# Kernel optimization log

Hardware: AMD Instinct MI355X
Metric: run time of the kernel (lower is better)

Reference implementation:

```python
import jax, jax.numpy as jnp
import numpy as np

NEG_SLOPE = 0.2  # PyG GATConv default negative_slope


def gat_layer(x, src, dst, W, a_src, a_dst, bias, concat, N):
    """PyG GATConv: h = xW; e_ij = LeakyReLU(a_src.h_j + a_dst.h_i);
    alpha = segment-softmax over incoming edges of i; out_i = sum_j alpha_ij h_j."""
    H, C = a_src.shape
    h = (x @ W).reshape(N, H, C)                      # [N,H,C]
    alpha_s = jnp.einsum('nhc,hc->nh', h, a_src)      # [N,H]
    alpha_d = jnp.einsum('nhc,hc->nh', h, a_dst)      # [N,H]
    e = jax.nn.leaky_relu(alpha_s[src] + alpha_d[dst], NEG_SLOPE)  # [E,H]
    # numerically-stable segment softmax over destination nodes
    m = jax.ops.segment_max(e, dst, num_segments=N)   # [N,H]
    e = jnp.exp(e - m[dst])
    denom = jax.ops.segment_sum(e, dst, num_segments=N)
    alpha = e / (denom[dst] + 1e-16)                  # [E,H]
    msg = h[src] * alpha[:, :, None]                  # [E,H,C]
    out = jax.ops.segment_sum(msg, dst, num_segments=N)  # [N,H,C]
    out = out.reshape(N, H * C) if concat else out.mean(axis=1)
    return out + bias


def setup_inputs() -> dict:
    key = jax.random.key(0)
    ks = jax.random.split(key, 12)
    N, E, F_IN, C, H = 50000, 800000, 512, 32, 8
    s = 0.05
    x = jax.random.normal(ks[0], (N, F_IN), dtype=jnp.float32)
    edge_index = jax.random.randint(ks[1], (2, E), 0, N, dtype=jnp.int64)
    W1 = jax.random.normal(ks[2], (F_IN, H * C), dtype=jnp.float32) * s
    as1 = jax.random.normal(ks[3], (H, C), dtype=jnp.float32) * s
    ad1 = jax.random.normal(ks[4], (H, C), dtype=jnp.float32) * s
    b1 = jnp.zeros((H * C,), dtype=jnp.float32)
    W2 = jax.random.normal(ks[5], (H * C, H * C), dtype=jnp.float32) * s
    as2 = jax.random.normal(ks[6], (H, C), dtype=jnp.float32) * s
    ad2 = jax.random.normal(ks[7], (H, C), dtype=jnp.float32) * s
    b2 = jnp.zeros((C,), dtype=jnp.float32)
    Wp = jax.random.normal(ks[8], (C, 1), dtype=jnp.float32) * s
    bp = jnp.zeros((1,), dtype=jnp.float32)
    return {"edge_index": edge_index, "x": x, "W1": W1, "as1": as1, "ad1": ad1,
            "b1": b1, "W2": W2, "as2": as2, "ad2": ad2, "b2": b2,
            "Wp": Wp, "bp": bp}


def reference(edge_index, x, W1, as1, ad1, b1, W2, as2, ad2, b2, Wp, bp):
    N = x.shape[0]
    # PyG GATConv adds self-loops by default
    loops = jnp.arange(N, dtype=edge_index.dtype)
    src = jnp.concatenate([edge_index[0], loops])
    dst = jnp.concatenate([edge_index[1], loops])
    h = gat_layer(x, src, dst, W1, as1, ad1, b1, concat=True, N=N)
    h = jax.nn.relu(h)
    # F.dropout(training=self.training) is identity in eval mode
    h = gat_layer(h, src, dst, W2, as2, ad2, b2, concat=False, N=N)
    return jax.nn.sigmoid(h @ Wp + bp)   # [N,1]
```

## Files before the change

### kernel.cpp

```cpp
#include <hip/hip_runtime.h>
#include <math.h>

#define H_HEADS 8
#define C_DIM   32
#define HC      256
#define F_IN    512
#define NEG_SLOPE 0.2f

typedef __attribute__((ext_vector_type(8))) short    bf16x8;
typedef __attribute__((ext_vector_type(4))) short    s16x4;
typedef __attribute__((ext_vector_type(4))) float    f32x4;
typedef __attribute__((ext_vector_type(2))) float    f32x2;

__device__ __forceinline__ short f2bf(float f) {
    union { float f; unsigned u; } v; v.f = f;
    unsigned r = v.u + 0x7FFF + ((v.u >> 16) & 1);
    return (short)(r >> 16);
}

__device__ __forceinline__ bf16x8 cvt8(float4 a, float4 b) {
    union { bf16x8 v; unsigned u[4]; } r;
    asm("v_cvt_pk_bf16_f32 %0, %1, %2" : "=v"(r.u[0]) : "v"(a.x), "v"(a.y));
    asm("v_cvt_pk_bf16_f32 %0, %1, %2" : "=v"(r.u[1]) : "v"(a.z), "v"(a.w));
    asm("v_cvt_pk_bf16_f32 %0, %1, %2" : "=v"(r.u[2]) : "v"(b.x), "v"(b.y));
    asm("v_cvt_pk_bf16_f32 %0, %1, %2" : "=v"(r.u[3]) : "v"(b.z), "v"(b.w));
    return r.v;
}

__device__ __forceinline__ void gl2lds16(const short* g, short* l) {
    __builtin_amdgcn_global_load_lds(
        (const __attribute__((address_space(1))) void*)g,
        (__attribute__((address_space(3))) void*)l, 16, 0, 0);
}

__global__ void wfrag_kernel(const float* __restrict__ W1, const float* __restrict__ W2,
                             short* __restrict__ Wf1, short* __restrict__ Wf2)
{
    const int NW1 = F_IN * HC;
    const int NW2 = HC * HC;
    int tid = blockIdx.x * 256 + threadIdx.x;
    const float* W; short* Wf; int t;
    if (tid < NW1)            { W = W1; Wf = Wf1; t = tid; }
    else if (tid < NW1 + NW2) { W = W2; Wf = Wf2; t = tid - NW1; }
    else return;
    int j  = t & 7;
    int l  = (t >> 3) & 63;
    int nb = (t >> 9) & 15;
    int s  = t >> 13;
    int k  = s * 32 + (l >> 4) * 8 + j;
    int n  = nb * 16 + (l & 15);
    Wf[t] = f2bf(W[(size_t)k * HC + n]);
}

template<bool ABF16>
__global__ __launch_bounds__(256) void gemm_mfma(const void* __restrict__ Aptr,
    const short* __restrict__ Bf, unsigned char* __restrict__ h8,
    const float* __restrict__ a_s, const float* __restrict__ a_d,
    float* __restrict__ alpha_s, float* __restrict__ alpha_d, int M, int K)
{
    __shared__ short Bs[2][8192];
    __shared__ float Als[512], Ald[512];

    const int tid  = threadIdx.x;
    const int w    = tid >> 6;
    const int lane = tid & 63;
    const int quad = lane >> 4;
    const int ml   = lane & 15;
    const int bm   = blockIdx.x * 64;

    const int rowA = bm + w * 16 + ml;
    const int rowL = rowA < M ? rowA : M - 1;

    f32x4 acc[16];
    #pragma unroll
    for (int nb = 0; nb < 16; ++nb) acc[nb] = (f32x4){0.f, 0.f, 0.f, 0.f};

    const float* A32 = (const float*)Aptr;
    const short* A16 = (const short*)Aptr;
    const int nsteps = K >> 5;

    {
        const short* g = Bf + (size_t)w * 2048 + lane * 8;
        short* l = &Bs[0][w * 2048];
        #pragma unroll
        for (int c = 0; c < 4; ++c) gl2lds16(g + c * 512, l + c * 512);
    }

    float4 p0, p1;
    bf16x8 pb;
    if (ABF16) {
        pb = *(const bf16x8*)(A16 + (size_t)rowL * K + quad * 8);
    } else {
        const float* ap = A32 + (size_t)rowL * K + quad * 8;
        p0 = *(const float4*)(ap);
        p1 = *(const float4*)(ap + 4);
    }

    for (int s = 0; s < nsteps; ++s) {
        __syncthreads();

        if (s + 1 < nsteps) {
            const short* g = Bf + (size_t)(s + 1) * 8192 + w * 2048 + lane * 8;
            short* l = &Bs[(s + 1) & 1][w * 2048];
            #pragma unroll
            for (int c = 0; c < 4; ++c) gl2lds16(g + c * 512, l + c * 512);
        }

        bf16x8 af;
        if (ABF16) {
            af = pb;
            if (s + 1 < nsteps)
                pb = *(const bf16x8*)(A16 + (size_t)rowL * K + (s + 1) * 32 + quad * 8);
        } else {
            af = cvt8(p0, p1);
            if (s + 1 < nsteps) {
                const float* ap = A32 + (size_t)rowL * K + (s + 1) * 32 + quad * 8;
                p0 = *(const float4*)(ap);
                p1 = *(const float4*)(ap + 4);
            }
        }

        const short* bsrc = &Bs[s & 1][lane * 8];
        #pragma unroll
        for (int nb = 0; nb < 16; ++nb) {
            bf16x8 bfr = *(const bf16x8*)(bsrc + nb * 512);
            acc[nb] = __builtin_amdgcn_mfma_f32_16x16x32_bf16(af, bfr, acc[nb], 0, 0, 0);
        }
    }

    float as_v[16], ad_v[16];
    #pragma unroll
    for (int nb = 0; nb < 16; ++nb) {
        as_v[nb] = a_s[nb * 16 + ml];
        ad_v[nb] = a_d[nb * 16 + ml];
    }

    #pragma unroll
    for (int r = 0; r < 4; ++r) {
        const int rl  = w * 16 + quad * 4 + r;
        const int row = bm + rl;

        if (row < M) {
            unsigned char* hrow = h8 + (size_t)row * HC;
            #pragma unroll
            for (int i = 0; i < 8; ++i) {
                int pk = __builtin_amdgcn_cvt_pk_fp8_f32(acc[2 * i][r], acc[2 * i + 1][r], 0, false);
                hrow[(2 * i) * 16 + ml]     = (unsigned char)(pk & 0xFF);
                hrow[(2 * i + 1) * 16 + ml] = (unsigned char)((pk >> 8) & 0xFF);
            }
        }

        float hs[8], hd[8];
        #pragma unroll
        for (int q = 0; q < 8; ++q) {
            hs[q] = acc[2 * q][r] * as_v[2 * q] + acc[2 * q + 1][r] * as_v[2 * q + 1];
            hd[q] = acc[2 * q][r] * ad_v[2 * q] + acc[2 * q + 1][r] * ad_v[2 * q + 1];
        }
        #pragma unroll
        for (int off = 1; off < 16; off <<= 1) {
            #pragma unroll
            for (int q = 0; q < 8; ++q) {
                hs[q] += __shfl_xor(hs[q], off);
                hd[q] += __shfl_xor(hd[q], off);
            }
        }
        if (ml == 0) {
            #pragma unroll
            for (int q = 0; q < 8; ++q) {
                Als[rl * 8 + q] = hs[q];
                Ald[rl * 8 + q] = hd[q];
            }
        }
    }
    __syncthreads();
    #pragma unroll
    for (int k = 0; k < 2; ++k) {
        int idx = tid + k * 256;
        int rl = idx >> 3, q = idx & 7;
        int row = bm + rl;
        if (row < M) {
            alpha_s[(size_t)row * H_HEADS + q] = Als[idx];
            alpha_d[(size_t)row * H_HEADS + q] = Ald[idx];
        }
    }
}

__global__ void zero_int(int* __restrict__ p, int n)
{
    int i = blockIdx.x * 256 + threadIdx.x;
    if (i < n) p[i] = 0;
}

__global__ void hist_kernel(const int* __restrict__ ei, int E, int N,
                            int* __restrict__ cnt)
{
    int e = blockIdx.x * 256 + threadIdx.x;
    if (e < E) atomicAdd(&cnt[ei[E + e]], 1);
    else if (e < E + N) atomicAdd(&cnt[e - E], 1);
}

__global__ __launch_bounds__(256) void scan_sum(const int* __restrict__ cnt, int n,
                                                int* __restrict__ chunk_sum)
{
    __shared__ int lds[256];
    int b = blockIdx.x, t = threadIdx.x;
    int base = b * 1024 + t * 4;
    int s = 0;
    #pragma unroll
    for (int j = 0; j < 4; ++j) { int i = base + j; if (i < n) s += cnt[i]; }
    lds[t] = s; __syncthreads();
    for (int off = 128; off > 0; off >>= 1) {
        if (t < off) lds[t] += lds[t + off];
        __syncthreads();
    }
    if (t == 0) chunk_sum[b] = lds[0];
}

__global__ __launch_bounds__(256) void scan_local(const int* __restrict__ cnt, int n,
    const int* __restrict__ chunk_sum, int nch, int* __restrict__ row_ptr)
{
    __shared__ int lds[256];
    int b = blockIdx.x, t = threadIdx.x;
    int lane = t & 63;

    int cs  = (lane < nch) ? chunk_sum[lane] : 0;
    int pre = (lane < b)   ? cs : 0;
    int tot = cs;
    #pragma unroll
    for (int off = 32; off > 0; off >>= 1) {
        pre += __shfl_xor(pre, off);
        tot += __shfl_xor(tot, off);
    }

    int base = b * 1024 + t * 4;
    int v[4]; int s = 0;
    #pragma unroll
    for (int j = 0; j < 4; ++j) { int i = base + j; v[j] = (i < n) ? cnt[i] : 0; s += v[j]; }
    lds[t] = s; __syncthreads();
    for (int off = 1; off < 256; off <<= 1) {
        int u = (t >= off) ? lds[t - off] : 0;
        __syncthreads();
        lds[t] += u;
        __syncthreads();
    }
    int run = lds[t] - s + pre;
    #pragma unroll
    for (int j = 0; j < 4; ++j) {
        int i = base + j;
        if (i < n) row_ptr[i] = run;
        run += v[j];
    }
    if (b == gridDim.x - 1 && t == 0) row_ptr[n] = tot;
}

__global__ void scatter_kernel(const int* __restrict__ ei, int E, int N,
    const int* __restrict__ row_ptr, int* __restrict__ cnt, int* __restrict__ es)
{
    int e = blockIdx.x * 256 + threadIdx.x;
    int src, dst;
    if (e < E)          { src = ei[e]; dst = ei[E + e]; }
    else if (e < E + N) { src = dst = e - E; }
    else return;
    int pos = row_ptr[dst] + atomicSub(&cnt[dst], 1) - 1;
    es[pos] = src;
}

#define ACC4(word, wgt, base_) do { \
    f32x2 lo_ = __builtin_amdgcn_cvt_pk_f32_fp8((word), false); \
    f32x2 hi_ = __builtin_amdgcn_cvt_pk_f32_fp8((word), true);  \
    acc[(base_) + 0] = fmaf((wgt), lo_[0], acc[(base_) + 0]); \
    acc[(base_) + 1] = fmaf((wgt), lo_[1], acc[(base_) + 1]); \
    acc[(base_) + 2] = fmaf((wgt), hi_[0], acc[(base_) + 2]); \
    acc[(base_) + 3] = fmaf((wgt), hi_[1], acc[(base_) + 3]); \
} while (0)

__device__ __forceinline__ float edge_w(float av, float ad8) {
    float e = av + ad8;
    return __expf(e > 0.f ? e : NEG_SLOPE * e);
}

__global__ __launch_bounds__(256) void agg1_kernel(const unsigned char* __restrict__ h8,
    const float* __restrict__ asb, const float* __restrict__ adb,
    const int* __restrict__ row_ptr, const int* __restrict__ es,
    const float* __restrict__ bias, short* __restrict__ z_bf, int N)
{
    const int l  = threadIdx.x & 63;
    const int i  = blockIdx.x * 4 + (threadIdx.x >> 6);
    if (i >= N) return;
    const int c  = l & 15;
    const int eo = l >> 4;
    const int hh = c >> 1;
    const float ad8 = adb[(size_t)i * 8 + hh];
    const int beg = row_ptr[i], end = row_ptr[i + 1];

    float acc[16];
    #pragma unroll
    for (int j = 0; j < 16; ++j) acc[j] = 0.f;
    float dsum = 0.f;

    int p = beg;
    for (; p + 7 < end; p += 8) {
        int s0 = es[p + eo], s1 = es[p + 4 + eo];
        float a0 = asb[(size_t)s0 * 8 + hh];
        float a1 = asb[(size_t)s1 * 8 + hh];
        uint4 h0 = *(const uint4*)(h8 + (size_t)s0 * 256 + c * 16);
        uint4 h1 = *(const uint4*)(h8 + (size_t)s1 * 256 + c * 16);
        float w0 = edge_w(a0, ad8);
        float w1 = edge_w(a1, ad8);
        ACC4(h0.x, w0, 0); ACC4(h0.y, w0, 4); ACC4(h0.z, w0, 8); ACC4(h0.w, w0, 12);
        ACC4(h1.x, w1, 0); ACC4(h1.y, w1, 4); ACC4(h1.z, w1, 8); ACC4(h1.w, w1, 12);
        dsum += w0 + w1;
    }
    for (; p < end; p += 4) {
        int pe = p + eo;
        int pc = pe < end ? pe : end - 1;
        int s0 = es[pc];
        float w0 = pe < end ? edge_w(asb[(size_t)s0 * 8 + hh], ad8) : 0.f;
        uint4 h0 = *(const uint4*)(h8 + (size_t)s0 * 256 + c * 16);
        ACC4(h0.x, w0, 0); ACC4(h0.y, w0, 4); ACC4(h0.z, w0, 8); ACC4(h0.w, w0, 12);
        dsum += w0;
    }

    #pragma unroll
    for (int j = 0; j < 16; ++j) {
        acc[j] += __shfl_xor(acc[j], 32);
        acc[j] += __shfl_xor(acc[j], 16);
    }
    dsum += __shfl_xor(dsum, 32);
    dsum += __shfl_xor(dsum, 16);

    float inv = 1.f / (dsum + 1e-16f);
    if (eo == 0) {
        union { short s[16]; bf16x8 v[2]; } zz;
        #pragma unroll
        for (int j = 0; j < 16; ++j) {
            float z = acc[j] * inv + bias[c * 16 + j];
            zz.s[j] = f2bf(z > 0.f ? z : 0.f);
        }
        *(bf16x8*)(z_bf + (size_t)i * HC + c * 16)     = zz.v[0];
        *(bf16x8*)(z_bf + (size_t)i * HC + c * 16 + 8) = zz.v[1];
    }
}

__global__ __launch_bounds__(256) void agg2_kernel(const unsigned char* __restrict__ h8,
    const float* __restrict__ asb, const float* __restrict__ adb,
    const int* __restrict__ row_ptr, const int* __restrict__ es,
    const float* __restrict__ b2, const float* __restrict__ Wp,
    const float* __restrict__ bp, float* __restrict__ out, int N)
{
    const int l  = threadIdx.x & 63;
    const int i  = blockIdx.x * 4 + (threadIdx.x >> 6);
    if (i >= N) return;
    const int c  = l & 15;
    const int eo = l >> 4;
    const int hh = c >> 1;
    const float ad8 = adb[(size_t)i * 8 + hh];
    const int beg = row_ptr[i], end = row_ptr[i + 1];

    float acc[16];
    #pragma unroll
    for (int j = 0; j < 16; ++j) acc[j] = 0.f;
    float dsum = 0.f;

    int p = beg;
    for (; p + 7 < end; p += 8) {
        int s0 = es[p + eo], s1 = es[p + 4 + eo];
        float a0 = asb[(size_t)s0 * 8 + hh];
        float a1 = asb[(size_t)s1 * 8 + hh];
        uint4 h0 = *(const uint4*)(h8 + (size_t)s0 * 256 + c * 16);
        uint4 h1 = *(const uint4*)(h8 + (size_t)s1 * 256 + c * 16);
        float w0 = edge_w(a0, ad8);
        float w1 = edge_w(a1, ad8);
        ACC4(h0.x, w0, 0); ACC4(h0.y, w0, 4); ACC4(h0.z, w0, 8); ACC4(h0.w, w0, 12);
        ACC4(h1.x, w1, 0); ACC4(h1.y, w1, 4); ACC4(h1.z, w1, 8); ACC4(h1.w, w1, 12);
        dsum += w0 + w1;
    }
    for (; p < end; p += 4) {
        int pe = p + eo;
        int pc = pe < end ? pe : end - 1;
        int s0 = es[pc];
        float w0 = pe < end ? edge_w(asb[(size_t)s0 * 8 + hh], ad8) : 0.f;
        uint4 h0 = *(const uint4*)(h8 + (size_t)s0 * 256 + c * 16);
        ACC4(h0.x, w0, 0); ACC4(h0.y, w0, 4); ACC4(h0.z, w0, 8); ACC4(h0.w, w0, 12);
        dsum += w0;
    }

    #pragma unroll
    for (int j = 0; j < 16; ++j) {
        acc[j] += __shfl_xor(acc[j], 32);
        acc[j] += __shfl_xor(acc[j], 16);
    }
    dsum += __shfl_xor(dsum, 32);
    dsum += __shfl_xor(dsum, 16);

    float inv = 1.f / (dsum + 1e-16f);
    const int wb = (c & 1) << 4;
    float partial = 0.f;
    #pragma unroll
    for (int j = 0; j < 16; ++j) partial = fmaf(acc[j] * inv, Wp[wb + j], partial);
    if (eo == 0 && c < 2) {
        #pragma unroll
        for (int j = 0; j < 16; ++j) partial += 8.f * b2[c * 16 + j] * Wp[c * 16 + j];
    }
    #pragma unroll
    for (int off = 8; off > 0; off >>= 1) partial += __shfl_xor(partial, off);
    if (l == 0) out[i] = 1.f / (1.f + __expf(-(0.125f * partial + bp[0])));
}

extern "C" void kernel_launch(void* const* d_in, const int* in_sizes, int n_in,
                              void* d_out, int out_size, void* d_ws, size_t ws_size,
                              hipStream_t stream)
{
    const int*   ei  = (const int*)d_in[0];
    const float* x   = (const float*)d_in[1];
    const float* W1  = (const float*)d_in[2];
    const float* as1 = (const float*)d_in[3];
    const float* ad1 = (const float*)d_in[4];
    const float* b1  = (const float*)d_in[5];
    const float* W2  = (const float*)d_in[6];
    const float* as2 = (const float*)d_in[7];
    const float* ad2 = (const float*)d_in[8];
    const float* b2  = (const float*)d_in[9];
    const float* Wp  = (const float*)d_in[10];
    const float* bp  = (const float*)d_in[11];
    float* out = (float*)d_out;

    const int E = in_sizes[0] / 2;
    const int N = in_sizes[1] / F_IN;
    const int ET = E + N;

    float*         asb = (float*)d_ws;
    float*         adb = asb + (size_t)N * H_HEADS;
    unsigned char* h8  = (unsigned char*)(adb + (size_t)N * H_HEADS);
    short*         z1b = (short*)(h8 + (size_t)N * HC);
    short*         Wf1 = z1b + (size_t)N * HC;
    short*         Wf2 = Wf1 + (size_t)F_IN * HC;
    int*           es  = (int*)(Wf2 + (size_t)HC * HC);
    int* cnt       = es + ET;
    int* row_ptr   = cnt + N;
    int* chunk_sum = row_ptr + N + 1;

    const int NCH = (N + 1023) / 1024;
    const int MB  = (N + 63) / 64;
    const int NB4 = (N + 3) / 4;

    zero_int<<<(N + 255) / 256, 256, 0, stream>>>(cnt, N);
    hist_kernel<<<(ET + 255) / 256, 256, 0, stream>>>(ei, E, N, cnt);
    scan_sum<<<NCH, 256, 0, stream>>>(cnt, N, chunk_sum);
    scan_local<<<NCH, 256, 0, stream>>>(cnt, N, chunk_sum, NCH, row_ptr);
    scatter_kernel<<<(ET + 255) / 256, 256, 0, stream>>>(ei, E, N, row_ptr, cnt, es);

    wfrag_kernel<<<(F_IN * HC + HC * HC + 255) / 256, 256, 0, stream>>>(W1, W2, Wf1, Wf2);

    gemm_mfma<false><<<MB, 256, 0, stream>>>(x, Wf1, h8, as1, ad1, asb, adb, N, F_IN);
    agg1_kernel<<<NB4, 256, 0, stream>>>(h8, asb, adb, row_ptr, es, b1, z1b, N);

    gemm_mfma<true><<<MB, 256, 0, stream>>>(z1b, Wf2, h8, as2, ad2, asb, adb, N, HC);
    agg2_kernel<<<NB4, 256, 0, stream>>>(h8, asb, adb, row_ptr, es, b2, Wp, bp, out, N);
}
```

Baseline: 404.5 us.

## Split GEMM output columns across two blocks to double grid size

The MFMA GEMM now assigns each block half of the 256 output columns (four heads) instead of all of them, doubling the number of blocks. Accumulators, LDS B buffers and alpha staging are halved. The aim is more parallelism and occupancy across the GPU's CUs, and lower register and LDS pressure. In exchange, each A row tile is loaded and converted twice, once per column half.

```diff
diff --git a/kernel.cpp b/kernel.cpp
--- a/kernel.cpp
+++ b/kernel.cpp
@@ -58,32 +58,33 @@
     const float* __restrict__ a_s, const float* __restrict__ a_d,
     float* __restrict__ alpha_s, float* __restrict__ alpha_d, int M, int K)
 {
-    __shared__ short Bs[2][8192];
-    __shared__ float Als[512], Ald[512];
+    __shared__ short Bs[2][4096];
+    __shared__ float Als[256], Ald[256];
 
     const int tid  = threadIdx.x;
     const int w    = tid >> 6;
     const int lane = tid & 63;
     const int quad = lane >> 4;
     const int ml   = lane & 15;
-    const int bm   = blockIdx.x * 64;
+    const int cb   = blockIdx.x & 1;
+    const int bm   = (blockIdx.x >> 1) * 64;
 
     const int rowA = bm + w * 16 + ml;
     const int rowL = rowA < M ? rowA : M - 1;
 
-    f32x4 acc[16];
-    #pragma unroll
-    for (int nb = 0; nb < 16; ++nb) acc[nb] = (f32x4){0.f, 0.f, 0.f, 0.f};
+    f32x4 acc[8];
+    #pragma unroll
+    for (int nb = 0; nb < 8; ++nb) acc[nb] = (f32x4){0.f, 0.f, 0.f, 0.f};
 
     const float* A32 = (const float*)Aptr;
     const short* A16 = (const short*)Aptr;
     const int nsteps = K >> 5;
 
     {
-        const short* g = Bf + (size_t)w * 2048 + lane * 8;
-        short* l = &Bs[0][w * 2048];
-        #pragma unroll
-        for (int c = 0; c < 4; ++c) gl2lds16(g + c * 512, l + c * 512);
+        const short* g = Bf + (size_t)cb * 4096 + w * 512 + lane * 8;
+        short* l = &Bs[0][w * 512 + lane * 8];
+        gl2lds16(g, l);
+        gl2lds16(g + 2048, l + 2048);
     }
 
     float4 p0, p1;
@@ -100,10 +101,10 @@
         __syncthreads();
 
         if (s + 1 < nsteps) {
-            const short* g = Bf + (size_t)(s + 1) * 8192 + w * 2048 + lane * 8;
-            short* l = &Bs[(s + 1) & 1][w * 2048];
-            #pragma unroll
-            for (int c = 0; c < 4; ++c) gl2lds16(g + c * 512, l + c * 512);
+            const short* g = Bf + (size_t)(s + 1) * 8192 + cb * 4096 + w * 512 + lane * 8;
+            short* l = &Bs[(s + 1) & 1][w * 512 + lane * 8];
+            gl2lds16(g, l);
+            gl2lds16(g + 2048, l + 2048);
         }
 
         bf16x8 af;
@@ -122,17 +123,17 @@
 
         const short* bsrc = &Bs[s & 1][lane * 8];
         #pragma unroll
-        for (int nb = 0; nb < 16; ++nb) {
+        for (int nb = 0; nb < 8; ++nb) {
             bf16x8 bfr = *(const bf16x8*)(bsrc + nb * 512);
             acc[nb] = __builtin_amdgcn_mfma_f32_16x16x32_bf16(af, bfr, acc[nb], 0, 0, 0);
         }
     }
 
-    float as_v[16], ad_v[16];
-    #pragma unroll
-    for (int nb = 0; nb < 16; ++nb) {
-        as_v[nb] = a_s[nb * 16 + ml];
-        ad_v[nb] = a_d[nb * 16 + ml];
+    float as_v[8], ad_v[8];
+    #pragma unroll
+    for (int nb = 0; nb < 8; ++nb) {
+        as_v[nb] = a_s[cb * 128 + nb * 16 + ml];
+        ad_v[nb] = a_d[cb * 128 + nb * 16 + ml];
     }
 
     #pragma unroll
@@ -141,46 +142,44 @@
         const int row = bm + rl;
 
         if (row < M) {
-            unsigned char* hrow = h8 + (size_t)row * HC;
+            unsigned char* hrow = h8 + (size_t)row * HC + cb * 128;
             #pragma unroll
-            for (int i = 0; i < 8; ++i) {
+            for (int i = 0; i < 4; ++i) {
                 int pk = __builtin_amdgcn_cvt_pk_fp8_f32(acc[2 * i][r], acc[2 * i + 1][r], 0, false);
                 hrow[(2 * i) * 16 + ml]     = (unsigned char)(pk & 0xFF);
                 hrow[(2 * i + 1) * 16 + ml] = (unsigned char)((pk >> 8) & 0xFF);
             }
         }
 
-        float hs[8], hd[8];
+        float hs[4], hd[4];
         #pragma unroll
-        for (int q = 0; q < 8; ++q) {
+        for (int q = 0; q < 4; ++q) {
             hs[q] = acc[2 * q][r] * as_v[2 * q] + acc[2 * q + 1][r] * as_v[2 * q + 1];
             hd[q] = acc[2 * q][r] * ad_v[2 * q] + acc[2 * q + 1][r] * ad_v[2 * q + 1];
         }
         #pragma unroll
         for (int off = 1; off < 16; off <<= 1) {
             #pragma unroll
-            for (int q = 0; q < 8; ++q) {
+            for (int q = 0; q < 4; ++q) {
                 hs[q] += __shfl_xor(hs[q], off);
                 hd[q] += __shfl_xor(hd[q], off);
             }
         }
         if (ml == 0) {
             #pragma unroll
-            for (int q = 0; q < 8; ++q) {
-                Als[rl * 8 + q] = hs[q];
-                Ald[rl * 8 + q] = hd[q];
+            for (int q = 0; q < 4; ++q) {
+                Als[rl * 4 + q] = hs[q];
+                Ald[rl * 4 + q] = hd[q];
             }
         }
     }
     __syncthreads();
-    #pragma unroll
-    for (int k = 0; k < 2; ++k) {
-        int idx = tid + k * 256;
-        int rl = idx >> 3, q = idx & 7;
+    {
+        int rl = tid >> 2, q = tid & 3;
         int row = bm + rl;
         if (row < M) {
-            alpha_s[(size_t)row * H_HEADS + q] = Als[idx];
-            alpha_d[(size_t)row * H_HEADS + q] = Ald[idx];
+            alpha_s[(size_t)row * H_HEADS + cb * 4 + q] = Als[tid];
+            alpha_d[(size_t)row * H_HEADS + cb * 4 + q] = Ald[tid];
         }
     }
 }
@@ -441,7 +440,7 @@
     int* chunk_sum = row_ptr + N + 1;
 
     const int NCH = (N + 1023) / 1024;
-    const int MB  = (N + 63) / 64;
+    const int MB  = ((N + 63) / 64) * 2;
     const int NB4 = (N + 3) / 4;
 
     zero_int<<<(N + 255) / 256, 256, 0, stream>>>(cnt, N);
```

Measured after the change: 399.8 us. About the same (-1.2%).
